# Optimization experiments

Hardware: AMD Instinct MI355X
Metric: run time of the kernel (lower is better)

The kernel has to match this reference:

```python
import jax, jax.numpy as jnp
import numpy as np


def setup_inputs() -> dict:
    key = jax.random.key(0)
    k1, k2 = jax.random.split(key)
    B, I, O = 16384, 1024, 4096
    return {
        "input": jax.random.normal(k1, (B, I), dtype=jnp.float32),
        "centers": jax.random.normal(k2, (O, I), dtype=jnp.float32),
        "log_sigma": jnp.zeros((O,), dtype=jnp.float32),
    }


def reference(input, centers, log_sigma):
    # as the torch broadcast-subtract-square-sum, without the (B,O,I) intermediate)
    x_sq = jnp.sum(input * input, axis=-1, keepdims=True)        # [B, 1]
    c_sq = jnp.sum(centers * centers, axis=-1)                   # [O]
    cross = input @ centers.T                                     # [B, O]
    d2 = jnp.maximum(x_sq + c_sq[None, :] - 2.0 * cross, 0.0)     # [B, O]
    sigma = jnp.exp(log_sigma)                                    # [O]
    return jnp.exp(-d2 / (2.0 * sigma * sigma)[None, :])
```

## Files before the change

kernel.cpp:

```cpp
#include <hip/hip_runtime.h>
#include <hip/hip_bf16.h>
#include <stdint.h>

#define TM 16384
#define TN 4096
#define TK 1024

#define BM 128
#define BN 128
#define BK 32

typedef __attribute__((ext_vector_type(8))) short bf16x8;
typedef __attribute__((ext_vector_type(4))) float f32x4;

static __device__ __forceinline__ ushort f2bf(float x) {
    __hip_bfloat16 h = __float2bfloat16(x);
    return *reinterpret_cast<ushort*>(&h);
}

__global__ __launch_bounds__(256) void rowsq_cvt(const float* __restrict__ src,
                                                 ushort* __restrict__ dst,
                                                 float* __restrict__ sq) {
    const int row = blockIdx.x;
    const int t = threadIdx.x;
    const size_t base = (size_t)row * TK + (size_t)t * 4;
    const float4 v = *(const float4*)(src + base);
    float s = v.x * v.x + v.y * v.y + v.z * v.z + v.w * v.w;

    ushort4 b;
    b.x = f2bf(v.x); b.y = f2bf(v.y); b.z = f2bf(v.z); b.w = f2bf(v.w);
    *(ushort4*)(dst + base) = b;

#pragma unroll
    for (int off = 32; off > 0; off >>= 1) s += __shfl_down(s, off);

    __shared__ float red[4];
    const int lane = t & 63, wave = t >> 6;
    if (lane == 0) red[wave] = s;
    __syncthreads();
    if (t == 0) sq[row] = red[0] + red[1] + red[2] + red[3];
}

__global__ __launch_bounds__(256) void scale_k(const float* __restrict__ ls,
                                               float* __restrict__ f) {
    const int i = blockIdx.x * 256 + threadIdx.x;
    if (i < TN) f[i] = -0.5f * expf(-2.0f * ls[i]);
}

__global__ __launch_bounds__(256) void rbf_gemm(const ushort* __restrict__ A,
                                                const ushort* __restrict__ B,
                                                const float* __restrict__ xsq,
                                                const float* __restrict__ csq,
                                                const float* __restrict__ fsc,
                                                float* __restrict__ out) {
    __shared__ __align__(16) ushort As[BM * BK];
    __shared__ __align__(16) ushort Bs[BN * BK];

    const int bn = blockIdx.x;
    const int bm = blockIdx.y;
    const int tid = threadIdx.x;
    const int lane = tid & 63, wave = tid >> 6;
    const int wr = wave >> 1, wc = wave & 1;
    const int lrow = lane & 15, lhi = lane >> 4;

    f32x4 acc[4][4];
#pragma unroll
    for (int m = 0; m < 4; ++m)
#pragma unroll
        for (int n = 0; n < 4; ++n)
            acc[m][n] = (f32x4){0.f, 0.f, 0.f, 0.f};

    const int srow = wave * 32 + (lane >> 2);
    const int scol = (lane & 3) * 8;
    const ushort* gA = A + (size_t)(bm * BM + srow) * TK + scol;
    const ushort* gB = B + (size_t)(bn * BN + srow) * TK + scol;
    ushort* lA = As + (size_t)(wave * 32) * BK;
    ushort* lB = Bs + (size_t)(wave * 32) * BK;

    for (int kt = 0; kt < TK; kt += BK) {
        __syncthreads();
        __builtin_amdgcn_global_load_lds(
            (const __attribute__((address_space(1))) void*)(gA + kt),
            (__attribute__((address_space(3))) void*)lA, 16, 0, 0);
        __builtin_amdgcn_global_load_lds(
            (const __attribute__((address_space(1))) void*)(gA + kt + 16 * TK),
            (__attribute__((address_space(3))) void*)(lA + 16 * BK), 16, 0, 0);
        __builtin_amdgcn_global_load_lds(
            (const __attribute__((address_space(1))) void*)(gB + kt),
            (__attribute__((address_space(3))) void*)lB, 16, 0, 0);
        __builtin_amdgcn_global_load_lds(
            (const __attribute__((address_space(1))) void*)(gB + kt + 16 * TK),
            (__attribute__((address_space(3))) void*)(lB + 16 * BK), 16, 0, 0);
        __syncthreads();

        bf16x8 af[4], bfr[4];
#pragma unroll
        for (int m = 0; m < 4; ++m)
            af[m] = *(const bf16x8*)(As + (wr * 64 + m * 16 + lrow) * BK + lhi * 8);
#pragma unroll
        for (int n = 0; n < 4; ++n)
            bfr[n] = *(const bf16x8*)(Bs + (wc * 64 + n * 16 + lrow) * BK + lhi * 8);

#pragma unroll
        for (int m = 0; m < 4; ++m)
#pragma unroll
            for (int n = 0; n < 4; ++n)
                acc[m][n] = __builtin_amdgcn_mfma_f32_16x16x32_bf16(
                    af[m], bfr[n], acc[m][n], 0, 0, 0);
    }

    const int row0 = bm * BM + wr * 64;
    const int col0 = bn * BN + wc * 64;
#pragma unroll
    for (int m = 0; m < 4; ++m) {
        const int rbase = row0 + m * 16 + lhi * 4;
        const float4 xs = *(const float4*)(xsq + rbase);
        const float xv[4] = {xs.x, xs.y, xs.z, xs.w};
#pragma unroll
        for (int n = 0; n < 4; ++n) {
            const int c = col0 + n * 16 + lrow;
            const float cs = csq[c];
            const float f = fsc[c];
#pragma unroll
            for (int j = 0; j < 4; ++j) {
                float d2 = xv[j] + cs - 2.0f * acc[m][n][j];
                d2 = fmaxf(d2, 0.0f);
                out[(size_t)(rbase + j) * TN + c] = __expf(f * d2);
            }
        }
    }
}

extern "C" void kernel_launch(void* const* d_in, const int* in_sizes, int n_in,
                              void* d_out, int out_size, void* d_ws, size_t ws_size,
                              hipStream_t stream) {
    const float* inp = (const float*)d_in[0];
    const float* ctr = (const float*)d_in[1];
    const float* ls  = (const float*)d_in[2];
    float* out = (float*)d_out;

    ushort* Abf = (ushort*)d_ws;
    ushort* Bbf = Abf + (size_t)TM * TK;
    float* xsq = (float*)(Bbf + (size_t)TN * TK);
    float* csq = xsq + TM;
    float* fsc = csq + TN;

    rowsq_cvt<<<TM, 256, 0, stream>>>(inp, Abf, xsq);
    rowsq_cvt<<<TN, 256, 0, stream>>>(ctr, Bbf, csq);
    scale_k<<<(TN + 255) / 256, 256, 0, stream>>>(ls, fsc);

    dim3 grid(TN / BN, TM / BM);
    rbf_gemm<<<grid, 256, 0, stream>>>(Abf, Bbf, xsq, csq, fsc, out);
}
```

Measured before the change: 223.1 us.

## Rewrite RBF GEMM as 256x256 double-buffered pipelined kernel with swizzled LDS

Replaces the 128x128x32 single-buffered GEMM with a 256x256 tile, BK=64, 512-thread kernel. LDS holds two stages, and global_load_lds prefetches are interleaved with MFMA phases using barriers, setprio and partial vmcnt waits. It also adds an XOR swizzle to avoid LDS bank conflicts and remaps block IDs for L2 locality. The aim is to hide load latency and raise MFMA utilization, at the cost of higher register and LDS use and fragile hand-written synchronization.

```diff
diff --git a/kernel.cpp b/kernel.cpp
--- a/kernel.cpp
+++ b/kernel.cpp
@@ -6,9 +6,7 @@
 #define TN 4096
 #define TK 1024
 
-#define BM 128
-#define BN 128
-#define BK 32
+#define NT (TK / 64)
 
 typedef __attribute__((ext_vector_type(8))) short bf16x8;
 typedef __attribute__((ext_vector_type(4))) float f32x4;
@@ -47,85 +45,161 @@
     if (i < TN) f[i] = -0.5f * expf(-2.0f * ls[i]);
 }
 
-__global__ __launch_bounds__(256) void rbf_gemm(const ushort* __restrict__ A,
+
+#define STAGE(PAN, G, T, H) do {                                               \
+    __builtin_amdgcn_global_load_lds(                                          \
+        (const __attribute__((address_space(1))) void*)((G) + (size_t)(H) * 128 * TK + (size_t)(T) * 64), \
+        (__attribute__((address_space(3))) void*)((PAN) + (H) * 8192 + wbase), \
+        16, 0, 0);                                                             \
+    __builtin_amdgcn_global_load_lds(                                          \
+        (const __attribute__((address_space(1))) void*)((G) + (size_t)(H) * 128 * TK + 64 * TK + (size_t)(T) * 64), \
+        (__attribute__((address_space(3))) void*)((PAN) + (H) * 8192 + 4096 + wbase), \
+        16, 0, 0);                                                             \
+} while (0)
+
+#define READA(PAN, QM) do {                                                    \
+    const ushort* _p = (PAN) + (size_t)(rowA + (QM) * 64) * 64 + cX;           \
+    _Pragma("unroll") for (int _i = 0; _i < 4; ++_i)                           \
+    _Pragma("unroll") for (int _k = 0; _k < 2; ++_k)                           \
+        af[_i][_k] = *(const bf16x8*)(_p + _i * 1024 + _k * 32);               \
+} while (0)
+
+#define READB(PAN, QN) do {                                                    \
+    const ushort* _p = (PAN) + (size_t)(rowB + (QN) * 32) * 64 + cX;           \
+    _Pragma("unroll") for (int _n = 0; _n < 2; ++_n)                           \
+    _Pragma("unroll") for (int _k = 0; _k < 2; ++_k)                           \
+        bf[(QN) * 2 + _n][_k] = *(const bf16x8*)(_p + _n * 1024 + _k * 32);    \
+} while (0)
+
+#define MFMA16(QM, QN)                                                         \
+    _Pragma("unroll") for (int _i = 0; _i < 4; ++_i)                           \
+    _Pragma("unroll") for (int _n = 0; _n < 2; ++_n)                           \
+    _Pragma("unroll") for (int _k = 0; _k < 2; ++_k)                           \
+        acc[(QM) * 4 + _i][(QN) * 2 + _n] =                                    \
+            __builtin_amdgcn_mfma_f32_16x16x32_bf16(                           \
+                af[_i][_k], bf[(QN) * 2 + _n][_k],                             \
+                acc[(QM) * 4 + _i][(QN) * 2 + _n], 0, 0, 0)
+
+#define PH_SYNC do {                                                           \
+    __builtin_amdgcn_s_barrier();                                              \
+    asm volatile("s_waitcnt lgkmcnt(0)" ::: "memory");                         \
+    __builtin_amdgcn_sched_barrier(0);                                         \
+    __builtin_amdgcn_s_setprio(1);                                             \
+} while (0)
+
+#define PH_END do {                                                            \
+    __builtin_amdgcn_s_setprio(0);                                             \
+    __builtin_amdgcn_s_barrier();                                              \
+} while (0)
+
+#define PH_END_VM do {                                                         \
+    __builtin_amdgcn_s_setprio(0);                                             \
+    asm volatile("s_waitcnt vmcnt(4)" ::: "memory");                           \
+    __builtin_amdgcn_s_barrier();                                              \
+} while (0)
+
+__global__ __launch_bounds__(512) void rbf_gemm(const ushort* __restrict__ A,
                                                 const ushort* __restrict__ B,
                                                 const float* __restrict__ xsq,
                                                 const float* __restrict__ csq,
                                                 const float* __restrict__ fsc,
                                                 float* __restrict__ out) {
-    __shared__ __align__(16) ushort As[BM * BK];
-    __shared__ __align__(16) ushort Bs[BN * BK];
-
-    const int bn = blockIdx.x;
-    const int bm = blockIdx.y;
+    __shared__ __align__(16) ushort lds[65536];
+
+    const int bid = blockIdx.x;
+    const int wg = (bid & 7) * 128 + (bid >> 3);
+    const int bm = wg >> 4;
+    const int bn = wg & 15;
+    const int row0 = bm * 256;
+    const int col0 = bn * 256;
+
     const int tid = threadIdx.x;
     const int lane = tid & 63, wave = tid >> 6;
-    const int wr = wave >> 1, wc = wave & 1;
+    const int wr = wave >> 2, wc = wave & 3;
     const int lrow = lane & 15, lhi = lane >> 4;
-
-    f32x4 acc[4][4];
-#pragma unroll
-    for (int m = 0; m < 4; ++m)
+    const int cX = (lhi * 8) ^ ((lrow & 4) << 2);
+    const int rowA = wr * 128 + lrow;
+    const int rowB = wc * 64 + lrow;
+    const int wbase = wave * 512;
+
+    const int srow = tid >> 3;
+    const int scol = ((tid & 7) * 8) ^ ((tid & 32) >> 1);
+    const ushort* gAl = A + (size_t)(row0 + srow) * TK + scol;
+    const ushort* gBl = B + (size_t)(col0 + srow) * TK + scol;
+
+    ushort* pA0 = lds;
+    ushort* pB0 = lds + 16384;
+    ushort* pA1 = lds + 32768;
+    ushort* pB1 = lds + 49152;
+
+    f32x4 acc[8][4];
+#pragma unroll
+    for (int m = 0; m < 8; ++m)
 #pragma unroll
         for (int n = 0; n < 4; ++n)
             acc[m][n] = (f32x4){0.f, 0.f, 0.f, 0.f};
 
-    const int srow = wave * 32 + (lane >> 2);
-    const int scol = (lane & 3) * 8;
-    const ushort* gA = A + (size_t)(bm * BM + srow) * TK + scol;
-    const ushort* gB = B + (size_t)(bn * BN + srow) * TK + scol;
-    ushort* lA = As + (size_t)(wave * 32) * BK;
-    ushort* lB = Bs + (size_t)(wave * 32) * BK;
-
-    for (int kt = 0; kt < TK; kt += BK) {
-        __syncthreads();
-        __builtin_amdgcn_global_load_lds(
-            (const __attribute__((address_space(1))) void*)(gA + kt),
-            (__attribute__((address_space(3))) void*)lA, 16, 0, 0);
-        __builtin_amdgcn_global_load_lds(
-            (const __attribute__((address_space(1))) void*)(gA + kt + 16 * TK),
-            (__attribute__((address_space(3))) void*)(lA + 16 * BK), 16, 0, 0);
-        __builtin_amdgcn_global_load_lds(
-            (const __attribute__((address_space(1))) void*)(gB + kt),
-            (__attribute__((address_space(3))) void*)lB, 16, 0, 0);
-        __builtin_amdgcn_global_load_lds(
-            (const __attribute__((address_space(1))) void*)(gB + kt + 16 * TK),
-            (__attribute__((address_space(3))) void*)(lB + 16 * BK), 16, 0, 0);
-        __syncthreads();
-
-        bf16x8 af[4], bfr[4];
-#pragma unroll
-        for (int m = 0; m < 4; ++m)
-            af[m] = *(const bf16x8*)(As + (wr * 64 + m * 16 + lrow) * BK + lhi * 8);
-#pragma unroll
-        for (int n = 0; n < 4; ++n)
-            bfr[n] = *(const bf16x8*)(Bs + (wc * 64 + n * 16 + lrow) * BK + lhi * 8);
-
-#pragma unroll
-        for (int m = 0; m < 4; ++m)
-#pragma unroll
-            for (int n = 0; n < 4; ++n)
-                acc[m][n] = __builtin_amdgcn_mfma_f32_16x16x32_bf16(
-                    af[m], bfr[n], acc[m][n], 0, 0, 0);
+    bf16x8 af[4][2];
+    bf16x8 bf[4][2];
+
+    STAGE(pB0, gBl, 0, 0); STAGE(pB0, gBl, 0, 1);
+    STAGE(pA0, gAl, 0, 0); STAGE(pA0, gAl, 0, 1);
+    STAGE(pB1, gBl, 1, 0); STAGE(pB1, gBl, 1, 1);
+    asm volatile("s_waitcnt vmcnt(4)" ::: "memory");
+    __builtin_amdgcn_s_barrier();
+
+#pragma unroll 1
+    for (int t = 0; t < NT; t += 2) {
+        const int T2 = (t + 2) & (NT - 1);
+        const int T3 = (t + 3) & (NT - 1);
+
+        READA(pA0, 0); READB(pB0, 0);
+        STAGE(pA1, gAl, t + 1, 0);
+        PH_SYNC; MFMA16(0, 0); PH_END;
+        READB(pB0, 1);
+        STAGE(pA1, gAl, t + 1, 1);
+        PH_SYNC; MFMA16(0, 1); PH_END;
+        READA(pA0, 1);
+        STAGE(pB0, gBl, T2, 0);
+        PH_SYNC; MFMA16(1, 0); PH_END;
+        STAGE(pB0, gBl, T2, 1);
+        PH_SYNC; MFMA16(1, 1); PH_END_VM;
+
+        READA(pA1, 0); READB(pB1, 0);
+        STAGE(pA0, gAl, T2, 0);
+        PH_SYNC; MFMA16(0, 0); PH_END;
+        READB(pB1, 1);
+        STAGE(pA0, gAl, T2, 1);
+        PH_SYNC; MFMA16(0, 1); PH_END;
+        READA(pA1, 1);
+        STAGE(pB1, gBl, T3, 0);
+        PH_SYNC; MFMA16(1, 0); PH_END;
+        STAGE(pB1, gBl, T3, 1);
+        PH_SYNC; MFMA16(1, 1); PH_END_VM;
     }
 
-    const int row0 = bm * BM + wr * 64;
-    const int col0 = bn * BN + wc * 64;
-#pragma unroll
-    for (int m = 0; m < 4; ++m) {
-        const int rbase = row0 + m * 16 + lhi * 4;
-        const float4 xs = *(const float4*)(xsq + rbase);
+    const int orow0 = row0 + wr * 128;
+    const int ocol0 = col0 + wc * 64;
+    float csv[4], fsv[4];
+    int cidx[4];
+#pragma unroll
+    for (int n = 0; n < 4; ++n) {
+        const int c = ocol0 + n * 16 + lrow;
+        cidx[n] = c;
+        csv[n] = csq[c];
+        fsv[n] = fsc[c];
+    }
+#pragma unroll
+    for (int m = 0; m < 8; ++m) {
+        const int rb = orow0 + m * 16 + lhi * 4;
+        const float4 xs = *(const float4*)(xsq + rb);
         const float xv[4] = {xs.x, xs.y, xs.z, xs.w};
 #pragma unroll
         for (int n = 0; n < 4; ++n) {
-            const int c = col0 + n * 16 + lrow;
-            const float cs = csq[c];
-            const float f = fsc[c];
 #pragma unroll
             for (int j = 0; j < 4; ++j) {
-                float d2 = xv[j] + cs - 2.0f * acc[m][n][j];
-                d2 = fmaxf(d2, 0.0f);
-                out[(size_t)(rbase + j) * TN + c] = __expf(f * d2);
+                float d2 = fmaxf(xv[j] + csv[n] - 2.0f * acc[m][n][j], 0.0f);
+                out[(size_t)(rb + j) * TN + cidx[n]] = __expf(fsv[n] * d2);
             }
         }
     }
@@ -149,6 +223,5 @@
     rowsq_cvt<<<TN, 256, 0, stream>>>(ctr, Bbf, csq);
     scale_k<<<(TN + 255) / 256, 256, 0, stream>>>(ls, fsc);
 
-    dim3 grid(TN / BN, TM / BM);
-    rbf_gemm<<<grid, 256, 0, stream>>>(Abf, Bbf, xsq, csq, fsc, out);
-}
+    rbf_gemm<<<(TM / 256) * (TN / 256), 512, 0, stream>>>(Abf, Bbf, xsq, csq, fsc, out);
+}
```

After: 185.1 us. -17.0%, faster.
